# Kernel optimization log

Measured on AMD Instinct MI355X. Metric: run time of the kernel, lower is better.

## Reference

```python
import jax, jax.numpy as jnp
import numpy as np

D_MODEL = 512
B, S = 4, 2048


def setup_inputs() -> dict:
    key = jax.random.key(0)
    ks = jax.random.split(key, 12)
    d = D_MODEL
    scale = 1.0 / np.sqrt(d)
    inp = {
        "query": jax.random.normal(ks[0], (B, S, d), dtype=jnp.float32),
        "key":   jax.random.normal(ks[1], (B, S, d), dtype=jnp.float32),
        "value": jax.random.normal(ks[2], (B, S, d), dtype=jnp.float32),
        "mask":  jax.random.uniform(ks[3], (B, S)) < 0.9,
        "num_heads": 8,
        "Wq": jax.random.normal(ks[4], (d, d), dtype=jnp.float32) * scale,
        "bq": jnp.zeros((d,), dtype=jnp.float32),
        "Wk": jax.random.normal(ks[5], (d, d), dtype=jnp.float32) * scale,
        "bk": jnp.zeros((d,), dtype=jnp.float32),
        "Wv": jax.random.normal(ks[6], (d, d), dtype=jnp.float32) * scale,
        "bv": jnp.zeros((d,), dtype=jnp.float32),
        "Wo": jax.random.normal(ks[7], (d, d), dtype=jnp.float32) * scale,
        "bo": jnp.zeros((d,), dtype=jnp.float32),
    }
    return inp


def _mha(query, key, value, mask, num_heads, Wq, bq, Wk, bk, Wv, bv, Wo, bo):
    b, s, d = query.shape
    h = num_heads
    dk = d // h
    # torch Linear: x @ W.T + b ; then split heads -> (b, h, s, dk)
    def proj(x, W, bias):
        return (x @ W.T + bias).reshape(b, s, h, dk).transpose(0, 2, 1, 3)
    q = proj(query, Wq, bq)
    k = proj(key, Wk, bk)
    v = proj(value, Wv, bv)
    scores = jnp.einsum('bhqd,bhkd->bhqk', q, k) / jnp.sqrt(jnp.float32(dk))
    # mask (b, s) broadcast over heads and query positions
    scores = jnp.where(mask[:, None, None, :], scores, -jnp.inf)
    attn = jax.nn.softmax(scores, axis=-1)
    # NaN fix: fully-masked rows produce NaN -> 0 (dropout is identity at eval)
    attn = jnp.where(jnp.isnan(attn), 0.0, attn)
    out = jnp.einsum('bhqk,bhkd->bhqd', attn, v)
    out = out.transpose(0, 2, 1, 3).reshape(b, s, d)
    output = out @ Wo.T + bo
    return output, attn.mean(axis=1)


def reference(query, key, value, mask, num_heads, Wq, bq, Wk, bk, Wv, bv, Wo, bo):
    return _mha(query, key, value, mask, num_heads, Wq, bq, Wk, bk, Wv, bv, Wo, bo)
```

## Files before the change

### kernel.cpp

```cpp
#include <hip/hip_runtime.h>
#include <cstdint>
#include <cstddef>

#define S_LEN 2048
#define D_MODEL 512
#define NHEAD 8
#define DKH 64
#define M_ROWS 8192

typedef unsigned short u16;
typedef unsigned int u32;
typedef short bf16x8 __attribute__((ext_vector_type(8)));
typedef float f32x4 __attribute__((ext_vector_type(4)));

#define MFMA16(a, b, c) __builtin_amdgcn_mfma_f32_16x16x32_bf16((a), (b), (c), 0, 0, 0)

__device__ __forceinline__ u16 f2bf(float f) {
  unsigned u = __float_as_uint(f);
  u += 0x7fffu + ((u >> 16) & 1u);
  return (u16)(u >> 16);
}
__device__ __forceinline__ u32 pack2bf(float f0, float f1) {
  return ((u32)f2bf(f1) << 16) | (u32)f2bf(f0);
}
__device__ __forceinline__ bf16x8 pack8(float4 a, float4 b) {
  union { u32 u[4]; bf16x8 v; } x;
  x.u[0] = pack2bf(a.x, a.y); x.u[1] = pack2bf(a.z, a.w);
  x.u[2] = pack2bf(b.x, b.y); x.u[3] = pack2bf(b.z, b.w);
  return x.v;
}

__global__ __launch_bounds__(512, 4) void proj_mfma(
    const float* __restrict__ X, const float* __restrict__ W,
    const float* __restrict__ bias, u16* __restrict__ Y, int mode)
{
  __shared__ __align__(16) u16 wlds[64 * 512];
  const int t = threadIdx.x;
  const int w = t >> 6, lane = t & 63, quad = lane >> 4, lq = lane & 15;
  const int n0 = blockIdx.x * 64;
  const int mb = blockIdx.y * 128 + w * 16;
  const int bb = mb >> 11, s0 = mb & 2047;
  const int h = n0 >> 6;

  for (int i = t; i < 4096; i += 512) {
    const int row = i >> 6, ck = i & 63;
    const float* p = W + (size_t)(n0 + row) * D_MODEL + ck * 8;
    *(bf16x8*)&wlds[(row * 512 + ck * 8) ^ ((row & 7) << 3)] =
        pack8(*(const float4*)p, *(const float4*)(p + 4));
  }

  bf16x8 xf[16];
  {
    const float* xr = X + (size_t)(mb + lq) * D_MODEL;
#pragma unroll
    for (int ks = 0; ks < 16; ++ks) {
      const float* p = xr + ks * 32 + quad * 8;
      xf[ks] = pack8(*(const float4*)p, *(const float4*)(p + 4));
    }
  }
  __syncthreads();

#pragma unroll
  for (int nt = 0; nt < 4; ++nt) {
    const int row = nt * 16 + lq;
    f32x4 acc = {0.f, 0.f, 0.f, 0.f};
#pragma unroll
    for (int ks = 0; ks < 16; ++ks) {
      const bf16x8 wf =
          *(const bf16x8*)&wlds[(row * 512 + ks * 32 + quad * 8) ^ ((row & 7) << 3)];
      acc = MFMA16(xf[ks], wf, acc);
    }
    const float bv = bias[n0 + nt * 16 + lq];
    if (mode == 0) {
#pragma unroll
      for (int r = 0; r < 4; ++r)
        Y[(((size_t)(bb * NHEAD + h) * S_LEN) + s0 + quad * 4 + r) * DKH + nt * 16 + lq] =
            f2bf(acc[r] + bv);
    } else {
      uint2 val;
      val.x = pack2bf(acc[0] + bv, acc[1] + bv);
      val.y = pack2bf(acc[2] + bv, acc[3] + bv);
      *(uint2*)&Y[(((size_t)(bb * NHEAD + h) * DKH) + nt * 16 + lq) * S_LEN + s0 + quad * 4] = val;
    }
  }
}

__global__ __launch_bounds__(512, 4) void attn_core(
    const float* __restrict__ Xin,
    const float* __restrict__ Wq, const float* __restrict__ bq,
    const u16* __restrict__ Kp, const u16* __restrict__ Vt,
    const int* __restrict__ mask,
    u16* __restrict__ Oh, float* __restrict__ lis, u16* __restrict__ Qp)
{
  __shared__ __align__(16) u16 kvb[2][2][4096];
  __shared__ __align__(16) u16 pst[8][16][72];
  __shared__ float gm[S_LEN];

  const int t = threadIdx.x;
  const int w = t >> 6, lane = t & 63, quad = lane >> 4, lq = lane & 15;
  const int srow = t >> 3, sblk = t & 7;
  const int bid = ((int)blockIdx.x & 7) * 64 + ((int)blockIdx.x >> 3);
  const int bb = bid >> 7, h = (bid >> 4) & 7, qc = bid & 15;
  const int qw = qc * 128 + w * 16;
  const size_t hB = (size_t)(bb * NHEAD + h) * S_LEN * DKH;
  const int sslot = srow * 64 + (sblk ^ (srow & 7)) * 8;

  for (int i = t; i < S_LEN; i += 512) gm[i] = mask[bb * S_LEN + i] ? 1.f : 0.f;

  uint4 rk = *(const uint4*)&Kp[hB + (size_t)srow * DKH + sblk * 8];
  uint4 rv = *(const uint4*)&Vt[hB + (size_t)srow * S_LEN + sblk * 8];

  {
    bf16x8 xf[16];
    const float* xr = Xin + (size_t)(bb * S_LEN + qw + lq) * D_MODEL;
#pragma unroll
    for (int ks = 0; ks < 16; ++ks) {
      const float* p = xr + ks * 32 + quad * 8;
      xf[ks] = pack8(*(const float4*)p, *(const float4*)(p + 4));
    }
#pragma unroll
    for (int nt = 0; nt < 4; ++nt) {
      f32x4 acc = {0.f, 0.f, 0.f, 0.f};
      for (int ks = 0; ks < 16; ++ks) {
        const float* wr = Wq + (size_t)(h * 64 + nt * 16 + lq) * D_MODEL + ks * 32 + quad * 8;
        acc = MFMA16(xf[ks], pack8(*(const float4*)wr, *(const float4*)(wr + 4)), acc);
      }
      const float bv = bq[h * 64 + nt * 16 + lq];
#pragma unroll
      for (int r = 0; r < 4; ++r) {
        const u16 qv = f2bf(acc[r] + bv);
        pst[w][quad * 4 + r][nt * 16 + lq] = qv;
        Qp[hB + (size_t)(qw + quad * 4 + r) * DKH + nt * 16 + lq] = qv;
      }
    }
  }
  bf16x8 qf[2];
#pragma unroll
  for (int ks = 0; ks < 2; ++ks)
    qf[ks] = *(const bf16x8*)&pst[w][lq][ks * 32 + quad * 8];

  *(uint4*)&kvb[0][0][sslot] = rk;
  *(uint4*)&kvb[0][1][sslot] = rv;
  rk = *(const uint4*)&Kp[hB + (size_t)(64 + srow) * DKH + sblk * 8];
  rv = *(const uint4*)&Vt[hB + (size_t)srow * S_LEN + 64 + sblk * 8];
  __syncthreads();

  f32x4 O[4];
#pragma unroll
  for (int dn = 0; dn < 4; ++dn) { f32x4 z = {0.f, 0.f, 0.f, 0.f}; O[dn] = z; }
  float ls[4] = {0.f, 0.f, 0.f, 0.f};
  const int rx = lq & 7;

#pragma unroll 1
  for (int kt = 0; kt < 32; ++kt) {
    const int c = kt & 1;
    if (kt + 1 < 32) {
      *(uint4*)&kvb[c ^ 1][0][sslot] = rk;
      *(uint4*)&kvb[c ^ 1][1][sslot] = rv;
    }
    if (kt + 2 < 32) {
      const int kb2 = (kt + 2) * 64;
      rk = *(const uint4*)&Kp[hB + (size_t)(kb2 + srow) * DKH + sblk * 8];
      rv = *(const uint4*)&Vt[hB + (size_t)srow * S_LEN + kb2 + sblk * 8];
    }
    const int kb = kt * 64;
    f32x4 p4[4];
    __builtin_amdgcn_s_setprio(1);
#pragma unroll
    for (int kn = 0; kn < 4; ++kn) {
      const bf16x8 k0 = *(const bf16x8*)&kvb[c][0][(kn * 16 + lq) * 64 + (quad ^ rx) * 8];
      const bf16x8 k1 = *(const bf16x8*)&kvb[c][0][(kn * 16 + lq) * 64 + ((4 + quad) ^ rx) * 8];
      f32x4 acc = {0.f, 0.f, 0.f, 0.f};
      acc = MFMA16(qf[0], k0, acc);
      acc = MFMA16(qf[1], k1, acc);
      p4[kn] = acc;
    }
    __builtin_amdgcn_s_setprio(0);
#pragma unroll
    for (int kn = 0; kn < 4; ++kn) {
      const float g = gm[kb + kn * 16 + lq];
#pragma unroll
      for (int r = 0; r < 4; ++r) {
        const float e = g * __expf(p4[kn][r] * 0.125f);
        ls[r] += e;
        pst[w][quad * 4 + r][kn * 16 + lq] = f2bf(e);
      }
    }
    bf16x8 pf0 = *(const bf16x8*)&pst[w][lq][quad * 8];
    bf16x8 pf1 = *(const bf16x8*)&pst[w][lq][32 + quad * 8];
    __builtin_amdgcn_s_setprio(1);
#pragma unroll
    for (int dn = 0; dn < 4; ++dn) {
      const bf16x8 v0 = *(const bf16x8*)&kvb[c][1][(dn * 16 + lq) * 64 + (quad ^ rx) * 8];
      const bf16x8 v1 = *(const bf16x8*)&kvb[c][1][(dn * 16 + lq) * 64 + ((4 + quad) ^ rx) * 8];
      O[dn] = MFMA16(pf0, v0, O[dn]);
      O[dn] = MFMA16(pf1, v1, O[dn]);
    }
    __builtin_amdgcn_s_setprio(0);
    __syncthreads();
  }

  float li[4];
#pragma unroll
  for (int r = 0; r < 4; ++r) {
    float v = ls[r];
    v += __shfl_xor(v, 1);
    v += __shfl_xor(v, 2);
    v += __shfl_xor(v, 4);
    v += __shfl_xor(v, 8);
    li[r] = (v > 0.f) ? 1.f / v : 0.f;
  }
  if (lq == 0) {
#pragma unroll
    for (int r = 0; r < 4; ++r)
      lis[(size_t)(bb * NHEAD + h) * S_LEN + qw + quad * 4 + r] = li[r];
  }
#pragma unroll
  for (int dn = 0; dn < 4; ++dn)
#pragma unroll
    for (int r = 0; r < 4; ++r)
      Oh[(size_t)(bb * S_LEN + qw + quad * 4 + r) * D_MODEL + h * 64 + dn * 16 + lq] =
          f2bf(O[dn][r] * li[r]);
}

__global__ __launch_bounds__(512, 4) void oproj_mfma(
    const u16* __restrict__ Oh, const float* __restrict__ W,
    const float* __restrict__ bias, float* __restrict__ out)
{
  __shared__ __align__(16) u16 wlds[64 * 512];
  const int t = threadIdx.x;
  const int w = t >> 6, lane = t & 63, quad = lane >> 4, lq = lane & 15;
  const int n0 = blockIdx.x * 64;
  const int mb = blockIdx.y * 128 + w * 16;

  for (int i = t; i < 4096; i += 512) {
    const int row = i >> 6, ck = i & 63;
    const float* p = W + (size_t)(n0 + row) * D_MODEL + ck * 8;
    *(bf16x8*)&wlds[(row * 512 + ck * 8) ^ ((row & 7) << 3)] =
        pack8(*(const float4*)p, *(const float4*)(p + 4));
  }

  bf16x8 xf[16];
#pragma unroll
  for (int ks = 0; ks < 16; ++ks)
    xf[ks] = *(const bf16x8*)&Oh[(size_t)(mb + lq) * D_MODEL + ks * 32 + quad * 8];
  __syncthreads();

#pragma unroll
  for (int nt = 0; nt < 4; ++nt) {
    const int row = nt * 16 + lq;
    f32x4 acc = {0.f, 0.f, 0.f, 0.f};
#pragma unroll
    for (int ks = 0; ks < 16; ++ks) {
      const bf16x8 wf =
          *(const bf16x8*)&wlds[(row * 512 + ks * 32 + quad * 8) ^ ((row & 7) << 3)];
      acc = MFMA16(xf[ks], wf, acc);
    }
    const float bv = bias[n0 + nt * 16 + lq];
#pragma unroll
    for (int r = 0; r < 4; ++r)
      out[(size_t)(mb + quad * 4 + r) * D_MODEL + n0 + nt * 16 + lq] = acc[r] + bv;
  }
}

__global__ __launch_bounds__(512, 4) void attn_mean(
    const u16* __restrict__ Qp, const u16* __restrict__ Kp,
    const float* __restrict__ lis, const int* __restrict__ mask,
    float* __restrict__ out1)
{
  __shared__ __align__(16) u16 qst[8][32][72];
  __shared__ float lfin[8][32];
  __shared__ float gm[S_LEN];

  const int t = threadIdx.x;
  const int w = t >> 6, lane = t & 63, quad = lane >> 4, lq = lane & 15;
  const int bid = ((int)blockIdx.x & 7) * 64 + ((int)blockIdx.x >> 3);
  const int bb = bid >> 7;
  const int q0 = ((bid >> 1) & 63) * 32;
  const int kh = bid & 1;
  const size_t bB = (size_t)bb * NHEAD * S_LEN * DKH;

  for (int i = t; i < S_LEN; i += 512) gm[i] = mask[bb * S_LEN + i] ? 1.f : 0.f;
  for (int i = t; i < 2048; i += 512) {
    const int h = i >> 8, qrow = (i >> 3) & 31, d8 = i & 7;
    *(uint4*)&qst[h][qrow][d8 * 8] =
        *(const uint4*)&Qp[bB + (size_t)h * S_LEN * DKH + (size_t)(q0 + qrow) * DKH + d8 * 8];
  }
  if (t < 256) {
    const int h = t >> 5, qr = t & 31;
    lfin[h][qr] = lis[(size_t)(bb * NHEAD + h) * S_LEN + q0 + qr];
  }
  __syncthreads();

  const int kc0 = kh * 1024 + w * 128;

#pragma unroll 1
  for (int kt = 0; kt < 2; ++kt) {
    const int kb = kc0 + kt * 64;
    float am[2][4][4];
#pragma unroll
    for (int qt = 0; qt < 2; ++qt)
#pragma unroll
      for (int kn = 0; kn < 4; ++kn)
#pragma unroll
        for (int r = 0; r < 4; ++r) am[qt][kn][r] = 0.f;

#pragma unroll 1
    for (int h = 0; h < 8; ++h) {
      const size_t hB = bB + (size_t)h * S_LEN * DKH;
      bf16x8 kf[8];
#pragma unroll
      for (int kn = 0; kn < 4; ++kn)
#pragma unroll
        for (int ks = 0; ks < 2; ++ks)
          kf[kn * 2 + ks] =
              *(const bf16x8*)&Kp[hB + (size_t)(kb + kn * 16 + lq) * DKH + ks * 32 + quad * 8];
#pragma unroll
      for (int qt = 0; qt < 2; ++qt) {
        const bf16x8 qh0 = *(const bf16x8*)&qst[h][qt * 16 + lq][quad * 8];
        const bf16x8 qh1 = *(const bf16x8*)&qst[h][qt * 16 + lq][32 + quad * 8];
        const float4 li4 = *(const float4*)&lfin[h][qt * 16 + quad * 4];
#pragma unroll
        for (int kn = 0; kn < 4; ++kn) {
          f32x4 acc = {0.f, 0.f, 0.f, 0.f};
          acc = MFMA16(qh0, kf[kn * 2 + 0], acc);
          acc = MFMA16(qh1, kf[kn * 2 + 1], acc);
          am[qt][kn][0] += __expf(acc[0] * 0.125f) * li4.x;
          am[qt][kn][1] += __expf(acc[1] * 0.125f) * li4.y;
          am[qt][kn][2] += __expf(acc[2] * 0.125f) * li4.z;
          am[qt][kn][3] += __expf(acc[3] * 0.125f) * li4.w;
        }
      }
    }
#pragma unroll
    for (int qt = 0; qt < 2; ++qt)
#pragma unroll
      for (int kn = 0; kn < 4; ++kn) {
        const float g8 = gm[kb + kn * 16 + lq] * 0.125f;
#pragma unroll
        for (int r = 0; r < 4; ++r)
          out1[((size_t)(bb * S_LEN + q0 + qt * 16 + quad * 4 + r)) * S_LEN + kb + kn * 16 + lq] =
              am[qt][kn][r] * g8;
      }
  }
}

__global__ void beacon_kernel(float* out, float val) { out[0] = val; }

extern "C" void kernel_launch(void* const* d_in, const int* in_sizes, int n_in,
                              void* d_out, int out_size, void* d_ws, size_t ws_size,
                              hipStream_t stream) {
  (void)in_sizes; (void)n_in; (void)out_size;
  const float* q  = (const float*)d_in[0];
  const float* k  = (const float*)d_in[1];
  const float* v  = (const float*)d_in[2];
  const int* mask = (const int*)d_in[3];
  const float* Wq = (const float*)d_in[5];
  const float* bq = (const float*)d_in[6];
  const float* Wk = (const float*)d_in[7];
  const float* bk = (const float*)d_in[8];
  const float* Wv = (const float*)d_in[9];
  const float* bv = (const float*)d_in[10];
  const float* Wo = (const float*)d_in[11];
  const float* bo = (const float*)d_in[12];

  float* out0 = (float*)d_out;
  float* out1 = out0 + (size_t)4 * S_LEN * D_MODEL;

  if (ws_size < (19ull << 20)) {
    beacon_kernel<<<1, 1, 0, stream>>>(out0, 100.0f + (float)(ws_size >> 20));
    return;
  }

  char* ws = (char*)d_ws;
  u16* Kp   = (u16*)(ws);
  u16* Vt   = (u16*)(ws + (8ull << 20));
  float* lis = (float*)(ws + (16ull << 20));
  u16* Qp   = (u16*)(ws + (17ull << 20));
  u16* Oh   = (u16*)out1;

  dim3 pg(D_MODEL / 64, M_ROWS / 128);
  proj_mfma<<<pg, 512, 0, stream>>>(k, Wk, bk, Kp, 0);
  proj_mfma<<<pg, 512, 0, stream>>>(v, Wv, bv, Vt, 1);

  attn_core<<<512, 512, 0, stream>>>(q, Wq, bq, Kp, Vt, mask, Oh, lis, Qp);
  oproj_mfma<<<pg, 512, 0, stream>>>(Oh, Wo, bo, out0);
  attn_mean<<<512, 512, 0, stream>>>(Qp, Kp, lis, mask, out1);
}
```

Baseline: 377.8 us.

## Pre-convert inputs and weights to bf16, merge Q/K/V projections into one launch

Adds a single batched conversion kernel that turns the fp32 activations and all four weight matrices into bf16, using the large attention-mean output buffer as scratch. The Q/K/V projections then run in one 3D-grid launch that loads bf16 directly, and the Q projection is moved out of attn_core, which now just reads the precomputed Qp. The goal is to avoid repeated fp32 weight reads and conversions in every block, especially the uncached Wq loads inside attn_core. In exchange there is an extra full pass over the inputs, plus the reliance on out1 as scratch before it is overwritten.

Measured after the change: 325.1 us. 14.0% less time.

```diff
diff --git a/kernel.cpp b/kernel.cpp
--- a/kernel.cpp
+++ b/kernel.cpp
@@ -30,11 +30,37 @@
   return x.v;
 }
 
-__global__ __launch_bounds__(512, 4) void proj_mfma(
-    const float* __restrict__ X, const float* __restrict__ W,
-    const float* __restrict__ bias, u16* __restrict__ Y, int mode)
+struct CvtArgs {
+  const float* src[7];
+  u16* dst[7];
+  int n8[7];
+};
+__global__ __launch_bounds__(256) void cvt_bf16(CvtArgs a) {
+  const int ai = blockIdx.y;
+  const float* __restrict__ s = a.src[ai];
+  u16* __restrict__ d = a.dst[ai];
+  const int n8 = a.n8[ai];
+  for (int i = blockIdx.x * 256 + threadIdx.x; i < n8; i += gridDim.x * 256) {
+    const float4 f0 = *(const float4*)&s[i * 8];
+    const float4 f1 = *(const float4*)&s[i * 8 + 4];
+    *(bf16x8*)&d[i * 8] = pack8(f0, f1);
+  }
+}
+
+__global__ __launch_bounds__(512, 4) void proj_qkv(
+    const u16* __restrict__ Xq, const u16* __restrict__ Xk, const u16* __restrict__ Xv,
+    const u16* __restrict__ Wqb, const u16* __restrict__ Wkb, const u16* __restrict__ Wvb,
+    const float* __restrict__ bq, const float* __restrict__ bk, const float* __restrict__ bv,
+    u16* __restrict__ Qp, u16* __restrict__ Kp, u16* __restrict__ Vt)
 {
   __shared__ __align__(16) u16 wlds[64 * 512];
+  const int z = blockIdx.z;
+  const u16* __restrict__ X = (z == 0) ? Xk : (z == 1) ? Xv : Xq;
+  const u16* __restrict__ W = (z == 0) ? Wkb : (z == 1) ? Wvb : Wqb;
+  const float* __restrict__ bias = (z == 0) ? bk : (z == 1) ? bv : bq;
+  u16* __restrict__ Y = (z == 0) ? Kp : (z == 1) ? Vt : Qp;
+  const int mode = (z == 1) ? 1 : 0;
+
   const int t = threadIdx.x;
   const int w = t >> 6, lane = t & 63, quad = lane >> 4, lq = lane & 15;
   const int n0 = blockIdx.x * 64;
@@ -44,20 +70,14 @@
 
   for (int i = t; i < 4096; i += 512) {
     const int row = i >> 6, ck = i & 63;
-    const float* p = W + (size_t)(n0 + row) * D_MODEL + ck * 8;
-    *(bf16x8*)&wlds[(row * 512 + ck * 8) ^ ((row & 7) << 3)] =
-        pack8(*(const float4*)p, *(const float4*)(p + 4));
+    *(uint4*)&wlds[(row * 512 + ck * 8) ^ ((row & 7) << 3)] =
+        *(const uint4*)&W[(size_t)(n0 + row) * D_MODEL + ck * 8];
   }
 
   bf16x8 xf[16];
-  {
-    const float* xr = X + (size_t)(mb + lq) * D_MODEL;
-#pragma unroll
-    for (int ks = 0; ks < 16; ++ks) {
-      const float* p = xr + ks * 32 + quad * 8;
-      xf[ks] = pack8(*(const float4*)p, *(const float4*)(p + 4));
-    }
-  }
+#pragma unroll
+  for (int ks = 0; ks < 16; ++ks)
+    xf[ks] = *(const bf16x8*)&X[(size_t)(mb + lq) * D_MODEL + ks * 32 + quad * 8];
   __syncthreads();
 
 #pragma unroll
@@ -70,27 +90,26 @@
           *(const bf16x8*)&wlds[(row * 512 + ks * 32 + quad * 8) ^ ((row & 7) << 3)];
       acc = MFMA16(xf[ks], wf, acc);
     }
-    const float bv = bias[n0 + nt * 16 + lq];
+    const float bv2 = bias[n0 + nt * 16 + lq];
     if (mode == 0) {
 #pragma unroll
       for (int r = 0; r < 4; ++r)
         Y[(((size_t)(bb * NHEAD + h) * S_LEN) + s0 + quad * 4 + r) * DKH + nt * 16 + lq] =
-            f2bf(acc[r] + bv);
+            f2bf(acc[r] + bv2);
     } else {
       uint2 val;
-      val.x = pack2bf(acc[0] + bv, acc[1] + bv);
-      val.y = pack2bf(acc[2] + bv, acc[3] + bv);
+      val.x = pack2bf(acc[0] + bv2, acc[1] + bv2);
+      val.y = pack2bf(acc[2] + bv2, acc[3] + bv2);
       *(uint2*)&Y[(((size_t)(bb * NHEAD + h) * DKH) + nt * 16 + lq) * S_LEN + s0 + quad * 4] = val;
     }
   }
 }
 
 __global__ __launch_bounds__(512, 4) void attn_core(
-    const float* __restrict__ Xin,
-    const float* __restrict__ Wq, const float* __restrict__ bq,
+    const u16* __restrict__ Qp,
     const u16* __restrict__ Kp, const u16* __restrict__ Vt,
     const int* __restrict__ mask,
-    u16* __restrict__ Oh, float* __restrict__ lis, u16* __restrict__ Qp)
+    u16* __restrict__ Oh, float* __restrict__ lis)
 {
   __shared__ __align__(16) u16 kvb[2][2][4096];
   __shared__ __align__(16) u16 pst[8][16][72];
@@ -110,34 +129,10 @@
   uint4 rk = *(const uint4*)&Kp[hB + (size_t)srow * DKH + sblk * 8];
   uint4 rv = *(const uint4*)&Vt[hB + (size_t)srow * S_LEN + sblk * 8];
 
-  {
-    bf16x8 xf[16];
-    const float* xr = Xin + (size_t)(bb * S_LEN + qw + lq) * D_MODEL;
-#pragma unroll
-    for (int ks = 0; ks < 16; ++ks) {
-      const float* p = xr + ks * 32 + quad * 8;
-      xf[ks] = pack8(*(const float4*)p, *(const float4*)(p + 4));
-    }
-#pragma unroll
-    for (int nt = 0; nt < 4; ++nt) {
-      f32x4 acc = {0.f, 0.f, 0.f, 0.f};
-      for (int ks = 0; ks < 16; ++ks) {
-        const float* wr = Wq + (size_t)(h * 64 + nt * 16 + lq) * D_MODEL + ks * 32 + quad * 8;
-        acc = MFMA16(xf[ks], pack8(*(const float4*)wr, *(const float4*)(wr + 4)), acc);
-      }
-      const float bv = bq[h * 64 + nt * 16 + lq];
-#pragma unroll
-      for (int r = 0; r < 4; ++r) {
-        const u16 qv = f2bf(acc[r] + bv);
-        pst[w][quad * 4 + r][nt * 16 + lq] = qv;
-        Qp[hB + (size_t)(qw + quad * 4 + r) * DKH + nt * 16 + lq] = qv;
-      }
-    }
-  }
   bf16x8 qf[2];
 #pragma unroll
   for (int ks = 0; ks < 2; ++ks)
-    qf[ks] = *(const bf16x8*)&pst[w][lq][ks * 32 + quad * 8];
+    qf[ks] = *(const bf16x8*)&Qp[hB + (size_t)(qw + lq) * DKH + ks * 32 + quad * 8];
 
   *(uint4*)&kvb[0][0][sslot] = rk;
   *(uint4*)&kvb[0][1][sslot] = rv;
@@ -224,7 +219,7 @@
 }
 
 __global__ __launch_bounds__(512, 4) void oproj_mfma(
-    const u16* __restrict__ Oh, const float* __restrict__ W,
+    const u16* __restrict__ Oh, const u16* __restrict__ Wb,
     const float* __restrict__ bias, float* __restrict__ out)
 {
   __shared__ __align__(16) u16 wlds[64 * 512];
@@ -235,9 +230,8 @@
 
   for (int i = t; i < 4096; i += 512) {
     const int row = i >> 6, ck = i & 63;
-    const float* p = W + (size_t)(n0 + row) * D_MODEL + ck * 8;
-    *(bf16x8*)&wlds[(row * 512 + ck * 8) ^ ((row & 7) << 3)] =
-        pack8(*(const float4*)p, *(const float4*)(p + 4));
+    *(uint4*)&wlds[(row * 512 + ck * 8) ^ ((row & 7) << 3)] =
+        *(const uint4*)&Wb[(size_t)(n0 + row) * D_MODEL + ck * 8];
   }
 
   bf16x8 xf[16];
@@ -373,17 +367,35 @@
   }
 
   char* ws = (char*)d_ws;
-  u16* Kp   = (u16*)(ws);
-  u16* Vt   = (u16*)(ws + (8ull << 20));
+  u16* Kp    = (u16*)(ws);
+  u16* Vt    = (u16*)(ws + (8ull << 20));
   float* lis = (float*)(ws + (16ull << 20));
-  u16* Qp   = (u16*)(ws + (17ull << 20));
-  u16* Oh   = (u16*)out1;
-
-  dim3 pg(D_MODEL / 64, M_ROWS / 128);
-  proj_mfma<<<pg, 512, 0, stream>>>(k, Wk, bk, Kp, 0);
-  proj_mfma<<<pg, 512, 0, stream>>>(v, Wv, bv, Vt, 1);
-
-  attn_core<<<512, 512, 0, stream>>>(q, Wq, bq, Kp, Vt, mask, Oh, lis, Qp);
-  oproj_mfma<<<pg, 512, 0, stream>>>(Oh, Wo, bo, out0);
+  u16* Qp    = (u16*)(ws + (17ull << 20));
+
+  char* o1 = (char*)out1;
+  u16* Oh    = (u16*)o1;
+  u16* Xq_bf = (u16*)(o1 + (8ull  << 20));
+  u16* Xk_bf = (u16*)(o1 + (16ull << 20));
+  u16* Xv_bf = (u16*)(o1 + (24ull << 20));
+  u16* Wq_bf = (u16*)(o1 + (32ull << 20));
+  u16* Wk_bf = Wq_bf + 262144;
+  u16* Wv_bf = Wk_bf + 262144;
+  u16* Wo_bf = Wv_bf + 262144;
+
+  CvtArgs ca;
+  ca.src[0] = q;  ca.dst[0] = Xq_bf; ca.n8[0] = M_ROWS * D_MODEL / 8;
+  ca.src[1] = k;  ca.dst[1] = Xk_bf; ca.n8[1] = M_ROWS * D_MODEL / 8;
+  ca.src[2] = v;  ca.dst[2] = Xv_bf; ca.n8[2] = M_ROWS * D_MODEL / 8;
+  ca.src[3] = Wq; ca.dst[3] = Wq_bf; ca.n8[3] = D_MODEL * D_MODEL / 8;
+  ca.src[4] = Wk; ca.dst[4] = Wk_bf; ca.n8[4] = D_MODEL * D_MODEL / 8;
+  ca.src[5] = Wv; ca.dst[5] = Wv_bf; ca.n8[5] = D_MODEL * D_MODEL / 8;
+  ca.src[6] = Wo; ca.dst[6] = Wo_bf; ca.n8[6] = D_MODEL * D_MODEL / 8;
+  cvt_bf16<<<dim3(256, 7), 256, 0, stream>>>(ca);
+
+  proj_qkv<<<dim3(8, 64, 3), 512, 0, stream>>>(
+      Xq_bf, Xk_bf, Xv_bf, Wq_bf, Wk_bf, Wv_bf, bq, bk, bv, Qp, Kp, Vt);
+
+  attn_core<<<512, 512, 0, stream>>>(Qp, Kp, Vt, mask, Oh, lis);
+  oproj_mfma<<<dim3(8, 64), 512, 0, stream>>>(Oh, Wo_bf, bo, out0);
   attn_mean<<<512, 512, 0, stream>>>(Qp, Kp, lis, mask, out1);
 }
```
